# Kernel optimization log

Hardware: AMD Instinct MI355X
Metric: run time of the kernel (lower is better)

The kernel has to match this reference:

```python
import jax, jax.numpy as jnp
import numpy as np

DIMS = 2048
HEADS = 16
HEAD_DIM = DIMS // HEADS  # 128
WIN = 256
THETA = 10000.0


def rotate_half(x):
    x1, x2 = jnp.split(x, 2, axis=-1)
    return jnp.concatenate([-x2, x1], axis=-1)


def rope_freqs(seq_len):
    inv_freq = 1.0 / (THETA ** (jnp.arange(0, HEAD_DIM, 2, dtype=jnp.float32) / HEAD_DIM))
    f = jnp.outer(jnp.arange(seq_len, dtype=jnp.float32), inv_freq)  # [S, D/2]
    return jnp.concatenate([f, f], axis=-1)[None, :, None, :]  # [1, S, 1, D]


def setup_inputs() -> dict:
    key = jax.random.key(0)
    ks = jax.random.split(key, 5)
    B, S = 2, 8192
    scale = 1.0 / np.sqrt(DIMS).astype(np.float32)
    return {
        "hidden_states": jax.random.normal(ks[0], (B, S, DIMS), jnp.float32),
        "Wq": jax.random.normal(ks[1], (DIMS, DIMS), jnp.float32) * scale,
        "Wk": jax.random.normal(ks[2], (DIMS, DIMS), jnp.float32) * scale,
        "Wv": jax.random.normal(ks[3], (DIMS, DIMS), jnp.float32) * scale,
        "Wo": jax.random.normal(ks[4], (DIMS, DIMS), jnp.float32) * scale,
    }


def reference(hidden_states, Wq, Wk, Wv, Wo):
    B, S, _ = hidden_states.shape
    # projections (weights stored [in, out])
    q = (hidden_states @ Wq).reshape(B, S, HEADS, HEAD_DIM)
    k = (hidden_states @ Wk).reshape(B, S, HEADS, HEAD_DIM)
    v = (hidden_states @ Wv).reshape(B, S, HEADS, HEAD_DIM)

    freqs = rope_freqs(S)
    cos, sin = jnp.cos(freqs), jnp.sin(freqs)
    q = q * cos + rotate_half(q) * sin
    k = k * cos + rotate_half(k) * sin

    C = S // WIN
    qc = q.reshape(B, C, WIN, HEADS, HEAD_DIM)
    kc = k.reshape(B, C, WIN, HEADS, HEAD_DIM)
    vc = v.reshape(B, C, WIN, HEADS, HEAD_DIM)

    # previous chunk's K/V (zeros for chunk 0; masked out anyway)
    kp = jnp.concatenate([jnp.zeros_like(kc[:, :1]), kc[:, :-1]], axis=1)
    vp = jnp.concatenate([jnp.zeros_like(vc[:, :1]), vc[:, :-1]], axis=1)
    kcat = jnp.concatenate([kp, kc], axis=2)  # [B, C, 2W, H, D]
    vcat = jnp.concatenate([vp, vc], axis=2)

    scores = jnp.einsum('bcqhd,bckhd->bchqk', qc, kcat) / np.float32(np.sqrt(HEAD_DIM))

    causal = jnp.tril(jnp.ones((WIN, WIN), dtype=bool))  # current-chunk causal
    prev_ok = (jnp.arange(C) > 0)[:, None, None]  # chunk 0 has no previous chunk
    mask = jnp.concatenate([
        jnp.broadcast_to(prev_ok, (C, WIN, WIN)),
        jnp.broadcast_to(causal[None], (C, WIN, WIN)),
    ], axis=-1)  # [C, W, 2W]

    scores = jnp.where(mask[None, :, None], scores, -jnp.inf)
    probs = jax.nn.softmax(scores, axis=-1)
    out = jnp.einsum('bchqk,bckhd->bcqhd', probs, vcat)
    out = out.reshape(B, S, DIMS)
    return out @ Wo
```

## Files before the change

kernel.cpp:

```cpp
#include <hip/hip_runtime.h>
#include <cmath>

#define DIMS 2048
#define SEQ  8192
#define NB   2
#define HEADS 16
#define HD   128
#define WINW 256
#define MROWS 16384
#define NCH  32

using bf16x8 = __attribute__((ext_vector_type(8))) short;
using f32x4  = __attribute__((ext_vector_type(4))) float;

__device__ __forceinline__ unsigned short f2bf(float f) {
  unsigned int u = __float_as_uint(f);
  u += 0x7FFF + ((u >> 16) & 1);
  return (unsigned short)(u >> 16);
}

__device__ __forceinline__ void async16(const unsigned short* g, unsigned short* l) {
  __builtin_amdgcn_global_load_lds((const __attribute__((address_space(1))) void*)g,
                                   (__attribute__((address_space(3))) void*)l,
                                   16, 0, 0);
}

#define BAR() __builtin_amdgcn_s_barrier()
#define WAIT_LGKM0() do { asm volatile("s_waitcnt lgkmcnt(0)" ::: "memory"); \
                          __builtin_amdgcn_sched_barrier(0); } while (0)
#define WAIT_VM(n) asm volatile("s_waitcnt vmcnt(" #n ")" ::: "memory")
#define MFMA16(a, b, c) __builtin_amdgcn_mfma_f32_16x16x32_bf16(a, b, c, 0, 0, 0)

__global__ __launch_bounds__(256) void prep(
    const float* __restrict__ w0, const float* __restrict__ w1,
    const float* __restrict__ w2, const float* __restrict__ w3,
    const float* __restrict__ H,
    unsigned short* __restrict__ Wt, unsigned short* __restrict__ Hb,
    float* __restrict__ cosT, float* __restrict__ sinT) {
  __shared__ unsigned short tile[64][65];
  const int bid = blockIdx.x;
  const int t = threadIdx.x;
  if (bid < 4096) {
    const int z = bid & 3;
    const int rest = bid >> 2;
    const int n0 = (rest & 31) * 64, k0 = (rest >> 5) * 64;
    const float* W = (z == 0) ? w0 : (z == 1) ? w1 : (z == 2) ? w2 : w3;
    unsigned short* O = Wt + (size_t)z * DIMS * DIMS;
    #pragma unroll
    for (int p = 0; p < 16; ++p) {
      int i = p * 4 + (t >> 6);
      int j = t & 63;
      tile[i][j] = f2bf(W[(size_t)(k0 + i) * DIMS + n0 + j]);
    }
    __syncthreads();
    #pragma unroll
    for (int p = 0; p < 16; ++p) {
      int a = p * 4 + (t >> 6);
      int b = t & 63;
      O[(size_t)(n0 + a) * DIMS + k0 + b] = tile[b][a];
    }
  } else if (bid < 6144) {
    const long n4 = (long)MROWS * DIMS / 4;
    long i = (long)(bid - 4096) * 256 + t;
    for (; i < n4; i += 524288) {
      float4 v = ((const float4*)H)[i];
      ushort4 o;
      o.x = f2bf(v.x); o.y = f2bf(v.y); o.z = f2bf(v.z); o.w = f2bf(v.w);
      ((ushort4*)Hb)[i] = o;
    }
  } else {
    int tl = (bid - 6144) * 256 + t;
    int pos = tl >> 6, i = tl & 63;
    double inv = pow(10000.0, -(double)i / 64.0);
    double ang = (double)pos * inv;
    cosT[tl] = (float)cos(ang);
    sinT[tl] = (float)sin(ang);
  }
}

template<int MODE>
__global__ __launch_bounds__(512, 2) void gemm256(
    const unsigned short* __restrict__ A,
    const unsigned short* __restrict__ WtAll,
    unsigned short* __restrict__ OutB,
    float* __restrict__ OutF,
    const float* __restrict__ cosT,
    const float* __restrict__ sinT) {
  __shared__ __align__(1024) unsigned short lds[65536];
  unsigned short* const As0 = lds;
  unsigned short* const Bs0 = lds + 16384;
  unsigned short* const As1 = lds + 32768;
  unsigned short* const Bs1 = lds + 49152;

  const int tid = threadIdx.x;
  const int wid = tid >> 6, lane = tid & 63;
  const int lo = lane & 15, hi = lane >> 4;
  const int wm = wid >> 2, wn = wid & 3;
  const int flip = (lo & 7) << 4;

  const int nwg = gridDim.x;
  const int orig = blockIdx.x;
  const int bid = (orig & 7) * (nwg >> 3) + (orig >> 3);

  int by, bx, z;
  if (MODE == 0) {
    z = bid >> 9;
    by = (bid & 511) >> 3;
    bx = bid & 7;
  } else {
    by = bid >> 3; bx = bid & 7; z = 3;
  }
  const int m0 = by * 256, n0 = bx * 256;
  const unsigned short* const Ag = A;
  const unsigned short* const Bg = WtAll + (size_t)z * DIMS * DIMS;

  f32x4 acc[8][4];
  #pragma unroll
  for (int i = 0; i < 8; ++i)
    #pragma unroll
    for (int j = 0; j < 4; ++j)
      acc[i][j] = (f32x4){0.f, 0.f, 0.f, 0.f};

  auto stage_half = [&](const unsigned short* __restrict__ G, int grow0, int tile,
                        unsigned short* dst) {
    const int k0 = tile * 64;
    #pragma unroll
    for (int h8 = 0; h8 < 2; ++h8) {
      const int c = h8 * 8 + wid;
      const int row = c * 8 + (lane >> 3);
      const int col8 = (lane & 7) ^ (lane >> 3);
      async16(G + (size_t)(grow0 + row) * DIMS + k0 + col8 * 8, dst + c * 512);
    }
  };
  auto rdA = [&](const unsigned short* base, int i, int kk) -> bf16x8 {
    const int r = i * 32 + wm * 16 + lo;
    const int cb = (kk * 64 + hi * 16) ^ flip;
    return *(const bf16x8*)((const char*)base + r * 128 + cb);
  };
  auto rdB = [&](const unsigned short* base, int j, int kk) -> bf16x8 {
    const int r = j * 64 + wn * 16 + lo;
    const int cb = (kk * 64 + hi * 16) ^ flip;
    return *(const bf16x8*)((const char*)base + r * 128 + cb);
  };

  bf16x8 aq[4][2], b0[2][2], b1[2][2];

  stage_half(Ag, m0,       0, As0);
  stage_half(Bg, n0,       0, Bs0);
  stage_half(Ag, m0 + 128, 0, As0 + 8192);
  stage_half(Bg, n0 + 128, 0, Bs0 + 8192);
  stage_half(Ag, m0,       1, As1);
  stage_half(Bg, n0,       1, Bs1);
  stage_half(Bg, n0 + 128, 1, Bs1 + 8192);
  WAIT_VM(6);
  BAR();

  #pragma unroll 1
  for (int it = 0; it < 16; ++it) {
    const int t = 2 * it;
    const bool pre = (it < 15);
    #pragma unroll
    for (int i = 0; i < 4; ++i) { aq[i][0] = rdA(As0, i, 0); aq[i][1] = rdA(As0, i, 1); }
    #pragma unroll
    for (int j = 0; j < 2; ++j) { b0[j][0] = rdB(Bs0, j, 0); b0[j][1] = rdB(Bs0, j, 1); }
    stage_half(Ag, m0 + 128, t + 1, As1 + 8192);
    WAIT_LGKM0();
    __builtin_amdgcn_s_setprio(1);
    #pragma unroll
    for (int kk = 0; kk < 2; ++kk)
      #pragma unroll
      for (int i = 0; i < 4; ++i)
        #pragma unroll
        for (int j = 0; j < 2; ++j)
          acc[i][j] = MFMA16(aq[i][kk], b0[j][kk], acc[i][j]);
    __builtin_amdgcn_s_setprio(0);
    BAR();
    #pragma unroll
    for (int j = 0; j < 2; ++j) { b1[j][0] = rdB(Bs0, 2 + j, 0); b1[j][1] = rdB(Bs0, 2 + j, 1); }
    if (pre) stage_half(Ag, m0, t + 2, As0);
    WAIT_LGKM0();
    __builtin_amdgcn_s_setprio(1);
    #pragma unroll
    for (int kk = 0; kk < 2; ++kk)
      #pragma unroll
      for (int i = 0; i < 4; ++i)
        #pragma unroll
        for (int j = 0; j < 2; ++j)
          acc[i][2 + j] = MFMA16(aq[i][kk], b1[j][kk], acc[i][2 + j]);
    __builtin_amdgcn_s_setprio(0);
    BAR();
    #pragma unroll
    for (int i = 0; i < 4; ++i) { aq[i][0] = rdA(As0, 4 + i, 0); aq[i][1] = rdA(As0, 4 + i, 1); }
    if (pre) stage_half(Bg, n0, t + 2, Bs0);
    WAIT_LGKM0();
    __builtin_amdgcn_s_setprio(1);
    #pragma unroll
    for (int kk = 0; kk < 2; ++kk)
      #pragma unroll
      for (int i = 0; i < 4; ++i)
        #pragma unroll
        for (int j = 0; j < 2; ++j)
          acc[4 + i][j] = MFMA16(aq[i][kk], b0[j][kk], acc[4 + i][j]);
    __builtin_amdgcn_s_setprio(0);
    BAR();
    if (pre) stage_half(Bg, n0 + 128, t + 2, Bs0 + 8192);
    __builtin_amdgcn_s_setprio(1);
    #pragma unroll
    for (int kk = 0; kk < 2; ++kk)
      #pragma unroll
      for (int i = 0; i < 4; ++i)
        #pragma unroll
        for (int j = 0; j < 2; ++j)
          acc[4 + i][2 + j] = MFMA16(aq[i][kk], b1[j][kk], acc[4 + i][2 + j]);
    __builtin_amdgcn_s_setprio(0);
    if (it == 15) { WAIT_VM(0); } else { WAIT_VM(6); }
    BAR();
    #pragma unroll
    for (int i = 0; i < 4; ++i) { aq[i][0] = rdA(As1, i, 0); aq[i][1] = rdA(As1, i, 1); }
    #pragma unroll
    for (int j = 0; j < 2; ++j) { b0[j][0] = rdB(Bs1, j, 0); b0[j][1] = rdB(Bs1, j, 1); }
    if (pre) stage_half(Ag, m0 + 128, t + 2, As0 + 8192);
    WAIT_LGKM0();
    __builtin_amdgcn_s_setprio(1);
    #pragma unroll
    for (int kk = 0; kk < 2; ++kk)
      #pragma unroll
      for (int i = 0; i < 4; ++i)
        #pragma unroll
        for (int j = 0; j < 2; ++j)
          acc[i][j] = MFMA16(aq[i][kk], b0[j][kk], acc[i][j]);
    __builtin_amdgcn_s_setprio(0);
    BAR();
    #pragma unroll
    for (int j = 0; j < 2; ++j) { b1[j][0] = rdB(Bs1, 2 + j, 0); b1[j][1] = rdB(Bs1, 2 + j, 1); }
    if (pre) stage_half(Ag, m0, t + 3, As1);
    WAIT_LGKM0();
    __builtin_amdgcn_s_setprio(1);
    #pragma unroll
    for (int kk = 0; kk < 2; ++kk)
      #pragma unroll
      for (int i = 0; i < 4; ++i)
        #pragma unroll
        for (int j = 0; j < 2; ++j)
          acc[i][2 + j] = MFMA16(aq[i][kk], b1[j][kk], acc[i][2 + j]);
    __builtin_amdgcn_s_setprio(0);
    BAR();
    #pragma unroll
    for (int i = 0; i < 4; ++i) { aq[i][0] = rdA(As1, 4 + i, 0); aq[i][1] = rdA(As1, 4 + i, 1); }
    if (pre) stage_half(Bg, n0, t + 3, Bs1);
    WAIT_LGKM0();
    __builtin_amdgcn_s_setprio(1);
    #pragma unroll
    for (int kk = 0; kk < 2; ++kk)
      #pragma unroll
      for (int i = 0; i < 4; ++i)
        #pragma unroll
        for (int j = 0; j < 2; ++j)
          acc[4 + i][j] = MFMA16(aq[i][kk], b0[j][kk], acc[4 + i][j]);
    __builtin_amdgcn_s_setprio(0);
    BAR();
    if (pre) stage_half(Bg, n0 + 128, t + 3, Bs1 + 8192);
    __builtin_amdgcn_s_setprio(1);
    #pragma unroll
    for (int kk = 0; kk < 2; ++kk)
      #pragma unroll
      for (int i = 0; i < 4; ++i)
        #pragma unroll
        for (int j = 0; j < 2; ++j)
          acc[4 + i][2 + j] = MFMA16(aq[i][kk], b1[j][kk], acc[4 + i][2 + j]);
    __builtin_amdgcn_s_setprio(0);
    WAIT_VM(6);
    BAR();
  }

  if (MODE == 0 && z == 2) {
    unsigned short* vt = OutB + (size_t)2 * MROWS * DIMS;
    #pragma unroll
    for (int i = 0; i < 8; ++i) {
      const int row0 = m0 + i * 32 + wm * 16 + hi * 4;
      const int bb = row0 >> 13;
      const int s0 = row0 & (SEQ - 1);
      #pragma unroll
      for (int j = 0; j < 4; ++j) {
        const int colg = n0 + j * 64 + wn * 16 + lo;
        ushort4 pk;
        pk.x = f2bf(acc[i][j][0]); pk.y = f2bf(acc[i][j][1]);
        pk.z = f2bf(acc[i][j][2]); pk.w = f2bf(acc[i][j][3]);
        *(ushort4*)&vt[(((size_t)(bb * 2048 + colg)) << 13) + s0] = pk;
      }
    }
  } else {
    unsigned short* outb = (MODE == 0) ? (OutB + (size_t)z * MROWS * DIMS)
                                       : (unsigned short*)nullptr;
    #pragma unroll
    for (int i = 0; i < 8; ++i) {
      #pragma unroll
      for (int rr = 0; rr < 4; ++rr) {
        const int row = m0 + i * 32 + wm * 16 + hi * 4 + rr;
        const int s = row & (SEQ - 1);
        if (MODE == 1) {
          float* o = OutF + (size_t)row * DIMS + n0;
          #pragma unroll
          for (int j = 0; j < 4; ++j) o[j * 64 + wn * 16 + lo] = acc[i][j][rr];
        } else {
          unsigned short* o = outb + (size_t)row * DIMS + n0;
          const int d = wn * 16 + lo;
          const float cc = cosT[s * 64 + d], sn = sinT[s * 64 + d];
          #pragma unroll
          for (int p = 0; p < 2; ++p) {
            const float v1 = acc[i][2 * p][rr], v2 = acc[i][2 * p + 1][rr];
            o[p * 128 + d]      = f2bf(v1 * cc - v2 * sn);
            o[p * 128 + d + 64] = f2bf(v2 * cc + v1 * sn);
          }
        }
      }
    }
  }
}

__global__ __launch_bounds__(512) void attn(
    const unsigned short* __restrict__ Qb,
    const unsigned short* __restrict__ Kb,
    const unsigned short* __restrict__ Vt,
    unsigned short* __restrict__ AO) {
  __shared__ unsigned short Ksm[2][64 * 128];
  __shared__ unsigned short Vsm[2][128 * 64];
  __shared__ unsigned short Psm[8 * 32 * 72];

  const int bid = blockIdx.x;
  const int h = bid & 15;
  const int c = (bid >> 4) & 31;
  const int b = bid >> 9;
  const int tid = threadIdx.x;
  const int wid = tid >> 6, lane = tid & 63;
  const int lo = lane & 15, hi = lane >> 4;
  const float SCALE = 0.08838834764831845f;

  bf16x8 qf[2][4];
  {
    const size_t base = ((size_t)(b * SEQ + c * WINW + wid * 32 + lo)) * DIMS + h * HD;
    #pragma unroll
    for (int m = 0; m < 2; ++m)
      #pragma unroll
      for (int ks = 0; ks < 4; ++ks)
        qf[m][ks] = *(const bf16x8*)&Qb[base + (size_t)m * 16 * DIMS + ks * 32 + hi * 8];
  }

  f32x4 O[2][8];
  float mrow[2][4], lrow[2][4];
  #pragma unroll
  for (int m = 0; m < 2; ++m) {
    #pragma unroll
    for (int n = 0; n < 8; ++n) O[m][n] = (f32x4){0.f, 0.f, 0.f, 0.f};
    #pragma unroll
    for (int r = 0; r < 4; ++r) { mrow[m][r] = -INFINITY; lrow[m][r] = 0.f; }
  }

  unsigned short* Pw = Psm + wid * 32 * 72;
  const int t0 = (c == 0) ? 4 : 0;

  const unsigned short* Kg0 = Kb + ((size_t)(b * SEQ + (c - 1) * WINW)) * DIMS + h * HD;
  const unsigned short* Vg0 = Vt + (((size_t)(b * 2048 + h * HD)) << 13) + (c - 1) * WINW;

  auto stageKV = [&](int t, int pb) {
    #pragma unroll
    for (int p = 0; p < 2; ++p) {
      const int cid = p * 512 + tid;
      const int row = cid >> 4, c16 = cid & 15;
      async16(Kg0 + (size_t)(t * 64 + row) * DIMS + ((c16 ^ (row & 7)) << 3),
              &Ksm[pb][cid * 8]);
    }
    #pragma unroll
    for (int p = 0; p < 2; ++p) {
      const int cid = p * 512 + tid;
      const int rd = cid >> 3, c8 = cid & 7;
      async16(Vg0 + ((size_t)rd << 13) + t * 64 + ((c8 ^ (rd & 7)) << 3),
              &Vsm[pb][cid * 8]);
    }
  };

  stageKV(t0, t0 & 1);
  for (int t = t0; t < 8; ++t) {
    const int pb = t & 1;
    if (t < 7) { stageKV(t + 1, pb ^ 1); WAIT_VM(4); } else { WAIT_VM(0); }
    BAR();

    const bool active = (t < 4) || (((t - 4) << 6) <= wid * 32 + 31);
    if (active) {
      f32x4 S[2][4];
      #pragma unroll
      for (int m = 0; m < 2; ++m)
        #pragma unroll
        for (int n = 0; n < 4; ++n)
          S[m][n] = (f32x4){0.f, 0.f, 0.f, 0.f};
      const char* Kbase = (const char*)&Ksm[pb][0];
      #pragma unroll
      for (int ks = 0; ks < 4; ++ks) {
        bf16x8 kf[4];
        #pragma unroll
        for (int n = 0; n < 4; ++n)
          kf[n] = *(const bf16x8*)(Kbase + (n * 16 + lo) * 256 +
                                   (((ks * 4 + hi) ^ (lo & 7)) << 4));
        #pragma unroll
        for (int m = 0; m < 2; ++m)
          #pragma unroll
          for (int n = 0; n < 4; ++n)
            S[m][n] = MFMA16(qf[m][ks], kf[n], S[m][n]);
      }

      float tmax[2][4];
      #pragma unroll
      for (int m = 0; m < 2; ++m) {
        #pragma unroll
        for (int r = 0; r < 4; ++r) {
          const int qrow = wid * 32 + m * 16 + hi * 4 + r;
          float tm = -INFINITY;
          #pragma unroll
          for (int n = 0; n < 4; ++n) {
            const int kc = t * 64 + n * 16 + lo;
            float v = S[m][n][r] * SCALE;
            const bool ok = (kc < WINW) ? (c > 0) : ((kc - WINW) <= qrow);
            v = ok ? v : -INFINITY;
            S[m][n][r] = v;
            tm = fmaxf(tm, v);
          }
          tm = fmaxf(tm, __shfl_xor(tm, 1));
          tm = fmaxf(tm, __shfl_xor(tm, 2));
          tm = fmaxf(tm, __shfl_xor(tm, 4));
          tm = fmaxf(tm, __shfl_xor(tm, 8));
          tmax[m][r] = tm;
        }
      }
      float need = -INFINITY;
      #pragma unroll
      for (int m = 0; m < 2; ++m)
        #pragma unroll
        for (int r = 0; r < 4; ++r)
          need = fmaxf(need, tmax[m][r] - mrow[m][r]);
      const bool fast = __all(need <= 8.0f);

      #pragma unroll
      for (int m = 0; m < 2; ++m) {
        #pragma unroll
        for (int r = 0; r < 4; ++r) {
          float mused = mrow[m][r];
          if (!fast) {
            mused = fmaxf(mused, tmax[m][r]);
            const float corr = __expf(mrow[m][r] - mused);
            lrow[m][r] *= corr;
            #pragma unroll
            for (int n = 0; n < 8; ++n) O[m][n][r] *= corr;
            mrow[m][r] = mused;
          }
          float rsum = 0.f;
          #pragma unroll
          for (int n = 0; n < 4; ++n) {
            const float p = __expf(S[m][n][r] - mused);
            S[m][n][r] = p;
            rsum += p;
          }
          rsum += __shfl_xor(rsum, 1);
          rsum += __shfl_xor(rsum, 2);
          rsum += __shfl_xor(rsum, 4);
          rsum += __shfl_xor(rsum, 8);
          lrow[m][r] += rsum;
          #pragma unroll
          for (int n = 0; n < 4; ++n)
            Pw[(m * 16 + hi * 4 + r) * 72 + n * 16 + lo] = f2bf(S[m][n][r]);
        }
      }
      asm volatile("" ::: "memory");

      const char* Vbase = (const char*)&Vsm[pb][0];
      #pragma unroll
      for (int kk = 0; kk < 2; ++kk) {
        const int ko = kk * 32 + hi * 8;
        bf16x8 pf[2], vf[8];
        #pragma unroll
        for (int m = 0; m < 2; ++m)
          pf[m] = *(const bf16x8*)&Pw[(m * 16 + lo) * 72 + ko];
        #pragma unroll
        for (int n = 0; n < 8; ++n)
          vf[n] = *(const bf16x8*)(Vbase + (n * 16 + lo) * 128 +
                                   (((kk * 4 + hi) ^ (lo & 7)) << 4));
        #pragma unroll
        for (int m = 0; m < 2; ++m)
          #pragma unroll
          for (int n = 0; n < 8; ++n)
            O[m][n] = MFMA16(pf[m], vf[n], O[m][n]);
      }
    }
    BAR();
  }

  #pragma unroll
  for (int m = 0; m < 2; ++m) {
    #pragma unroll
    for (int r = 0; r < 4; ++r) {
      const float inv = 1.f / lrow[m][r];
      const size_t row = (size_t)(b * SEQ + c * WINW + wid * 32 + m * 16 + hi * 4 + r);
      unsigned short* o = AO + row * DIMS + h * HD;
      #pragma unroll
      for (int n = 0; n < 8; ++n)
        o[n * 16 + lo] = f2bf(O[m][n][r] * inv);
    }
  }
}

extern "C" void kernel_launch(void* const* d_in, const int* in_sizes, int n_in,
                              void* d_out, int out_size, void* d_ws, size_t ws_size,
                              hipStream_t stream) {
  const float* H  = (const float*)d_in[0];
  const float* Wq = (const float*)d_in[1];
  const float* Wk = (const float*)d_in[2];
  const float* Wv = (const float*)d_in[3];
  const float* Wo = (const float*)d_in[4];
  float* out = (float*)d_out;

  unsigned short* Wt  = (unsigned short*)d_ws;
  unsigned short* Hb  = Wt + (size_t)4 * DIMS * DIMS;
  unsigned short* QKV = Hb + (size_t)MROWS * DIMS;
  unsigned short* AO  = QKV + (size_t)3 * MROWS * DIMS;
  float* cosT = (float*)(AO + (size_t)MROWS * DIMS);
  float* sinT = cosT + (size_t)SEQ * 64;

  prep<<<8192, 256, 0, stream>>>(Wq, Wk, Wv, Wo, H, Wt, Hb, cosT, sinT);
  gemm256<0><<<1536, 512, 0, stream>>>(Hb, Wt, QKV, nullptr, cosT, sinT);
  attn<<<dim3(1024), 512, 0, stream>>>(QKV, QKV + (size_t)MROWS * DIMS,
                                       QKV + (size_t)2 * MROWS * DIMS, AO);
  gemm256<1><<<512, 512, 0, stream>>>(AO, Wt, nullptr, out, cosT, sinT);
}
```

Measured before the change: 710.0 us.

## Split GEMM LDS waits per k-half and split attention blocks by query half

In the GEMM main loop, each LDS fragment read is split into two k-halves. Partial lgkmcnt waits let the first half of the MFMAs start while the second half is still loading. The attention kernel changes from 512-thread blocks over a whole chunk to 256-thread blocks over half the query rows, with a grid remap across groups of 8. Each query-half block loops only over the key tiles it needs, which cuts wasted causal iterations. The P scratch buffer drops its padding and uses an XOR swizzle to avoid bank conflicts. Smaller blocks with occupancy 2 raise parallelism but reload K/V for each half.

```diff
diff --git a/kernel.cpp b/kernel.cpp
--- a/kernel.cpp
+++ b/kernel.cpp
@@ -28,6 +28,9 @@
 #define BAR() __builtin_amdgcn_s_barrier()
 #define WAIT_LGKM0() do { asm volatile("s_waitcnt lgkmcnt(0)" ::: "memory"); \
                           __builtin_amdgcn_sched_barrier(0); } while (0)
+#define WAIT_LGKM(n) do { asm volatile("s_waitcnt lgkmcnt(" #n ")" ::: "memory"); \
+                          __builtin_amdgcn_sched_barrier(0); } while (0)
+#define ORDER() asm volatile("" ::: "memory")
 #define WAIT_VM(n) asm volatile("s_waitcnt vmcnt(" #n ")" ::: "memory")
 #define MFMA16(a, b, c) __builtin_amdgcn_mfma_f32_16x16x32_bf16(a, b, c, 0, 0, 0)
 
@@ -160,47 +163,70 @@
     const int t = 2 * it;
     const bool pre = (it < 15);
     #pragma unroll
-    for (int i = 0; i < 4; ++i) { aq[i][0] = rdA(As0, i, 0); aq[i][1] = rdA(As0, i, 1); }
-    #pragma unroll
-    for (int j = 0; j < 2; ++j) { b0[j][0] = rdB(Bs0, j, 0); b0[j][1] = rdB(Bs0, j, 1); }
+    for (int i = 0; i < 4; ++i) aq[i][0] = rdA(As0, i, 0);
+    #pragma unroll
+    for (int j = 0; j < 2; ++j) b0[j][0] = rdB(Bs0, j, 0);
+    ORDER();
+    #pragma unroll
+    for (int i = 0; i < 4; ++i) aq[i][1] = rdA(As0, i, 1);
+    #pragma unroll
+    for (int j = 0; j < 2; ++j) b0[j][1] = rdB(Bs0, j, 1);
     stage_half(Ag, m0 + 128, t + 1, As1 + 8192);
+    WAIT_LGKM(6);
+    __builtin_amdgcn_s_setprio(1);
+    #pragma unroll
+    for (int i = 0; i < 4; ++i)
+      #pragma unroll
+      for (int j = 0; j < 2; ++j)
+        acc[i][j] = MFMA16(aq[i][0], b0[j][0], acc[i][j]);
     WAIT_LGKM0();
-    __builtin_amdgcn_s_setprio(1);
-    #pragma unroll
-    for (int kk = 0; kk < 2; ++kk)
-      #pragma unroll
-      for (int i = 0; i < 4; ++i)
-        #pragma unroll
-        for (int j = 0; j < 2; ++j)
-          acc[i][j] = MFMA16(aq[i][kk], b0[j][kk], acc[i][j]);
-    __builtin_amdgcn_s_setprio(0);
-    BAR();
-    #pragma unroll
-    for (int j = 0; j < 2; ++j) { b1[j][0] = rdB(Bs0, 2 + j, 0); b1[j][1] = rdB(Bs0, 2 + j, 1); }
+    #pragma unroll
+    for (int i = 0; i < 4; ++i)
+      #pragma unroll
+      for (int j = 0; j < 2; ++j)
+        acc[i][j] = MFMA16(aq[i][1], b0[j][1], acc[i][j]);
+    __builtin_amdgcn_s_setprio(0);
+    BAR();
+    #pragma unroll
+    for (int j = 0; j < 2; ++j) b1[j][0] = rdB(Bs0, 2 + j, 0);
+    ORDER();
+    #pragma unroll
+    for (int j = 0; j < 2; ++j) b1[j][1] = rdB(Bs0, 2 + j, 1);
     if (pre) stage_half(Ag, m0, t + 2, As0);
+    WAIT_LGKM(2);
+    __builtin_amdgcn_s_setprio(1);
+    #pragma unroll
+    for (int i = 0; i < 4; ++i)
+      #pragma unroll
+      for (int j = 0; j < 2; ++j)
+        acc[i][2 + j] = MFMA16(aq[i][0], b1[j][0], acc[i][2 + j]);
     WAIT_LGKM0();
-    __builtin_amdgcn_s_setprio(1);
-    #pragma unroll
-    for (int kk = 0; kk < 2; ++kk)
-      #pragma unroll
-      for (int i = 0; i < 4; ++i)
-        #pragma unroll
-        for (int j = 0; j < 2; ++j)
-          acc[i][2 + j] = MFMA16(aq[i][kk], b1[j][kk], acc[i][2 + j]);
-    __builtin_amdgcn_s_setprio(0);
-    BAR();
-    #pragma unroll
-    for (int i = 0; i < 4; ++i) { aq[i][0] = rdA(As0, 4 + i, 0); aq[i][1] = rdA(As0, 4 + i, 1); }
+    #pragma unroll
+    for (int i = 0; i < 4; ++i)
+      #pragma unroll
+      for (int j = 0; j < 2; ++j)
+        acc[i][2 + j] = MFMA16(aq[i][1], b1[j][1], acc[i][2 + j]);
+    __builtin_amdgcn_s_setprio(0);
+    BAR();
+    #pragma unroll
+    for (int i = 0; i < 4; ++i) aq[i][0] = rdA(As0, 4 + i, 0);
+    ORDER();
+    #pragma unroll
+    for (int i = 0; i < 4; ++i) aq[i][1] = rdA(As0, 4 + i, 1);
     if (pre) stage_half(Bg, n0, t + 2, Bs0);
+    WAIT_LGKM(4);
+    __builtin_amdgcn_s_setprio(1);
+    #pragma unroll
+    for (int i = 0; i < 4; ++i)
+      #pragma unroll
+      for (int j = 0; j < 2; ++j)
+        acc[4 + i][j] = MFMA16(aq[i][0], b0[j][0], acc[4 + i][j]);
     WAIT_LGKM0();
-    __builtin_amdgcn_s_setprio(1);
-    #pragma unroll
-    for (int kk = 0; kk < 2; ++kk)
-      #pragma unroll
-      for (int i = 0; i < 4; ++i)
-        #pragma unroll
-        for (int j = 0; j < 2; ++j)
-          acc[4 + i][j] = MFMA16(aq[i][kk], b0[j][kk], acc[4 + i][j]);
+    #pragma unroll
+    for (int i = 0; i < 4; ++i)
+      #pragma unroll
+      for (int j = 0; j < 2; ++j)
+        acc[4 + i][j] = MFMA16(aq[i][1], b0[j][1], acc[4 + i][j]);
     __builtin_amdgcn_s_setprio(0);
     BAR();
     if (pre) stage_half(Bg, n0 + 128, t + 2, Bs0 + 8192);
@@ -216,47 +242,70 @@
     if (it == 15) { WAIT_VM(0); } else { WAIT_VM(6); }
     BAR();
     #pragma unroll
-    for (int i = 0; i < 4; ++i) { aq[i][0] = rdA(As1, i, 0); aq[i][1] = rdA(As1, i, 1); }
-    #pragma unroll
-    for (int j = 0; j < 2; ++j) { b0[j][0] = rdB(Bs1, j, 0); b0[j][1] = rdB(Bs1, j, 1); }
+    for (int i = 0; i < 4; ++i) aq[i][0] = rdA(As1, i, 0);
+    #pragma unroll
+    for (int j = 0; j < 2; ++j) b0[j][0] = rdB(Bs1, j, 0);
+    ORDER();
+    #pragma unroll
+    for (int i = 0; i < 4; ++i) aq[i][1] = rdA(As1, i, 1);
+    #pragma unroll
+    for (int j = 0; j < 2; ++j) b0[j][1] = rdB(Bs1, j, 1);
     if (pre) stage_half(Ag, m0 + 128, t + 2, As0 + 8192);
+    WAIT_LGKM(6);
+    __builtin_amdgcn_s_setprio(1);
+    #pragma unroll
+    for (int i = 0; i < 4; ++i)
+      #pragma unroll
+      for (int j = 0; j < 2; ++j)
+        acc[i][j] = MFMA16(aq[i][0], b0[j][0], acc[i][j]);
     WAIT_LGKM0();
-    __builtin_amdgcn_s_setprio(1);
-    #pragma unroll
-    for (int kk = 0; kk < 2; ++kk)
-      #pragma unroll
-      for (int i = 0; i < 4; ++i)
-        #pragma unroll
-        for (int j = 0; j < 2; ++j)
-          acc[i][j] = MFMA16(aq[i][kk], b0[j][kk], acc[i][j]);
-    __builtin_amdgcn_s_setprio(0);
-    BAR();
-    #pragma unroll
-    for (int j = 0; j < 2; ++j) { b1[j][0] = rdB(Bs1, 2 + j, 0); b1[j][1] = rdB(Bs1, 2 + j, 1); }
+    #pragma unroll
+    for (int i = 0; i < 4; ++i)
+      #pragma unroll
+      for (int j = 0; j < 2; ++j)
+        acc[i][j] = MFMA16(aq[i][1], b0[j][1], acc[i][j]);
+    __builtin_amdgcn_s_setprio(0);
+    BAR();
+    #pragma unroll
+    for (int j = 0; j < 2; ++j) b1[j][0] = rdB(Bs1, 2 + j, 0);
+    ORDER();
+    #pragma unroll
+    for (int j = 0; j < 2; ++j) b1[j][1] = rdB(Bs1, 2 + j, 1);
     if (pre) stage_half(Ag, m0, t + 3, As1);
+    WAIT_LGKM(2);
+    __builtin_amdgcn_s_setprio(1);
+    #pragma unroll
+    for (int i = 0; i < 4; ++i)
+      #pragma unroll
+      for (int j = 0; j < 2; ++j)
+        acc[i][2 + j] = MFMA16(aq[i][0], b1[j][0], acc[i][2 + j]);
     WAIT_LGKM0();
-    __builtin_amdgcn_s_setprio(1);
-    #pragma unroll
-    for (int kk = 0; kk < 2; ++kk)
-      #pragma unroll
-      for (int i = 0; i < 4; ++i)
-        #pragma unroll
-        for (int j = 0; j < 2; ++j)
-          acc[i][2 + j] = MFMA16(aq[i][kk], b1[j][kk], acc[i][2 + j]);
-    __builtin_amdgcn_s_setprio(0);
-    BAR();
-    #pragma unroll
-    for (int i = 0; i < 4; ++i) { aq[i][0] = rdA(As1, 4 + i, 0); aq[i][1] = rdA(As1, 4 + i, 1); }
+    #pragma unroll
+    for (int i = 0; i < 4; ++i)
+      #pragma unroll
+      for (int j = 0; j < 2; ++j)
+        acc[i][2 + j] = MFMA16(aq[i][1], b1[j][1], acc[i][2 + j]);
+    __builtin_amdgcn_s_setprio(0);
+    BAR();
+    #pragma unroll
+    for (int i = 0; i < 4; ++i) aq[i][0] = rdA(As1, 4 + i, 0);
+    ORDER();
+    #pragma unroll
+    for (int i = 0; i < 4; ++i) aq[i][1] = rdA(As1, 4 + i, 1);
     if (pre) stage_half(Bg, n0, t + 3, Bs1);
+    WAIT_LGKM(4);
+    __builtin_amdgcn_s_setprio(1);
+    #pragma unroll
+    for (int i = 0; i < 4; ++i)
+      #pragma unroll
+      for (int j = 0; j < 2; ++j)
+        acc[4 + i][j] = MFMA16(aq[i][0], b0[j][0], acc[4 + i][j]);
     WAIT_LGKM0();
-    __builtin_amdgcn_s_setprio(1);
-    #pragma unroll
-    for (int kk = 0; kk < 2; ++kk)
-      #pragma unroll
-      for (int i = 0; i < 4; ++i)
-        #pragma unroll
-        for (int j = 0; j < 2; ++j)
-          acc[4 + i][j] = MFMA16(aq[i][kk], b0[j][kk], acc[4 + i][j]);
+    #pragma unroll
+    for (int i = 0; i < 4; ++i)
+      #pragma unroll
+      for (int j = 0; j < 2; ++j)
+        acc[4 + i][j] = MFMA16(aq[i][1], b0[j][1], acc[4 + i][j]);
     __builtin_amdgcn_s_setprio(0);
     BAR();
     if (pre) stage_half(Bg, n0 + 128, t + 3, Bs1 + 8192);
@@ -318,27 +367,33 @@
   }
 }
 
-__global__ __launch_bounds__(512) void attn(
+__global__ __launch_bounds__(256, 2) void attn(
     const unsigned short* __restrict__ Qb,
     const unsigned short* __restrict__ Kb,
     const unsigned short* __restrict__ Vt,
     unsigned short* __restrict__ AO) {
   __shared__ unsigned short Ksm[2][64 * 128];
   __shared__ unsigned short Vsm[2][128 * 64];
-  __shared__ unsigned short Psm[8 * 32 * 72];
-
-  const int bid = blockIdx.x;
-  const int h = bid & 15;
-  const int c = (bid >> 4) & 31;
-  const int b = bid >> 9;
+  __shared__ unsigned short Psm[4 * 32 * 64];
+
+  const int nwg = gridDim.x;
+  const int orig = blockIdx.x;
+  const int bid = (orig & 7) * (nwg >> 3) + (orig >> 3);
+
+  const int qh = bid & 1;
+  const int h = (bid >> 1) & 15;
+  const int c = (bid >> 5) & 31;
+  const int b = bid >> 10;
   const int tid = threadIdx.x;
   const int wid = tid >> 6, lane = tid & 63;
   const int lo = lane & 15, hi = lane >> 4;
   const float SCALE = 0.08838834764831845f;
 
+  const int qbase = qh * 128 + wid * 32;
+
   bf16x8 qf[2][4];
   {
-    const size_t base = ((size_t)(b * SEQ + c * WINW + wid * 32 + lo)) * DIMS + h * HD;
+    const size_t base = ((size_t)(b * SEQ + c * WINW + qbase + lo)) * DIMS + h * HD;
     #pragma unroll
     for (int m = 0; m < 2; ++m)
       #pragma unroll
@@ -356,23 +411,24 @@
     for (int r = 0; r < 4; ++r) { mrow[m][r] = -INFINITY; lrow[m][r] = 0.f; }
   }
 
-  unsigned short* Pw = Psm + wid * 32 * 72;
+  unsigned short* Pw = Psm + wid * 32 * 64;
   const int t0 = (c == 0) ? 4 : 0;
+  const int tend = 5 + 2 * qh;
 
   const unsigned short* Kg0 = Kb + ((size_t)(b * SEQ + (c - 1) * WINW)) * DIMS + h * HD;
   const unsigned short* Vg0 = Vt + (((size_t)(b * 2048 + h * HD)) << 13) + (c - 1) * WINW;
 
   auto stageKV = [&](int t, int pb) {
     #pragma unroll
-    for (int p = 0; p < 2; ++p) {
-      const int cid = p * 512 + tid;
+    for (int p = 0; p < 4; ++p) {
+      const int cid = p * 256 + tid;
       const int row = cid >> 4, c16 = cid & 15;
       async16(Kg0 + (size_t)(t * 64 + row) * DIMS + ((c16 ^ (row & 7)) << 3),
               &Ksm[pb][cid * 8]);
     }
     #pragma unroll
-    for (int p = 0; p < 2; ++p) {
-      const int cid = p * 512 + tid;
+    for (int p = 0; p < 4; ++p) {
+      const int cid = p * 256 + tid;
       const int rd = cid >> 3, c8 = cid & 7;
       async16(Vg0 + ((size_t)rd << 13) + t * 64 + ((c8 ^ (rd & 7)) << 3),
               &Vsm[pb][cid * 8]);
@@ -380,12 +436,12 @@
   };
 
   stageKV(t0, t0 & 1);
-  for (int t = t0; t < 8; ++t) {
+  for (int t = t0; t <= tend; ++t) {
     const int pb = t & 1;
-    if (t < 7) { stageKV(t + 1, pb ^ 1); WAIT_VM(4); } else { WAIT_VM(0); }
-    BAR();
-
-    const bool active = (t < 4) || (((t - 4) << 6) <= wid * 32 + 31);
+    if (t < tend) { stageKV(t + 1, pb ^ 1); WAIT_VM(8); } else { WAIT_VM(0); }
+    BAR();
+
+    const bool active = (t < 4) || (((t - 4) << 6) <= qbase + 31);
     if (active) {
       f32x4 S[2][4];
       #pragma unroll
@@ -413,7 +469,7 @@
       for (int m = 0; m < 2; ++m) {
         #pragma unroll
         for (int r = 0; r < 4; ++r) {
-          const int qrow = wid * 32 + m * 16 + hi * 4 + r;
+          const int qrow = qbase + m * 16 + hi * 4 + r;
           float tm = -INFINITY;
           #pragma unroll
           for (int n = 0; n < 4; ++n) {
@@ -464,9 +520,12 @@
           rsum += __shfl_xor(rsum, 4);
           rsum += __shfl_xor(rsum, 8);
           lrow[m][r] += rsum;
-          #pragma unroll
-          for (int n = 0; n < 4; ++n)
-            Pw[(m * 16 + hi * 4 + r) * 72 + n * 16 + lo] = f2bf(S[m][n][r]);
+          const int q = m * 16 + hi * 4 + r;
+          #pragma unroll
+          for (int n = 0; n < 4; ++n) {
+            const int boff = (q << 7) + (((n * 16 + lo) << 1) ^ ((q & 7) << 4));
+            *(unsigned short*)((char*)Pw + boff) = f2bf(S[m][n][r]);
+          }
         }
       }
       asm volatile("" ::: "memory");
@@ -474,11 +533,13 @@
       const char* Vbase = (const char*)&Vsm[pb][0];
       #pragma unroll
       for (int kk = 0; kk < 2; ++kk) {
-        const int ko = kk * 32 + hi * 8;
         bf16x8 pf[2], vf[8];
         #pragma unroll
-        for (int m = 0; m < 2; ++m)
-          pf[m] = *(const bf16x8*)&Pw[(m * 16 + lo) * 72 + ko];
+        for (int m = 0; m < 2; ++m) {
+          const int q = m * 16 + lo;
+          pf[m] = *(const bf16x8*)((const char*)Pw + (q << 7) +
+                                   (((kk * 4 + hi) << 4) ^ ((q & 7) << 4)));
+        }
         #pragma unroll
         for (int n = 0; n < 8; ++n)
           vf[n] = *(const bf16x8*)(Vbase + (n * 16 + lo) * 128 +
@@ -498,7 +559,7 @@
     #pragma unroll
     for (int r = 0; r < 4; ++r) {
       const float inv = 1.f / lrow[m][r];
-      const size_t row = (size_t)(b * SEQ + c * WINW + wid * 32 + m * 16 + hi * 4 + r);
+      const size_t row = (size_t)(b * SEQ + c * WINW + qbase + m * 16 + hi * 4 + r);
       unsigned short* o = AO + row * DIMS + h * HD;
       #pragma unroll
       for (int n = 0; n < 8; ++n)
@@ -526,7 +587,7 @@
 
   prep<<<8192, 256, 0, stream>>>(Wq, Wk, Wv, Wo, H, Wt, Hb, cosT, sinT);
   gemm256<0><<<1536, 512, 0, stream>>>(Hb, Wt, QKV, nullptr, cosT, sinT);
-  attn<<<dim3(1024), 512, 0, stream>>>(QKV, QKV + (size_t)MROWS * DIMS,
-                                       QKV + (size_t)2 * MROWS * DIMS, AO);
+  attn<<<2048, 256, 0, stream>>>(QKV, QKV + (size_t)MROWS * DIMS,
+                                 QKV + (size_t)2 * MROWS * DIMS, AO);
   gemm256<1><<<512, 512, 0, stream>>>(AO, Wt, nullptr, out, cosT, sinT);
 }
```

Measured after the change: 707.4 us. No clear change (-0.4%).
